# Optimization experiments

Measured on AMD Instinct MI355X. Metric: run time of the kernel, lower is better.

The kernel has to match this reference:

```python
import jax, jax.numpy as jnp
import numpy as np
import jax.lax as lax


def _log_bf_np(z, s2, s0):
    # Bayes factor per feature; s0 is the prior precision tau_0[l,k] (scalar)
    s0_inv = 1.0 / s0
    s2ps0inv = s2 + s0_inv
    return 0.5 * (jnp.log(s2) - jnp.log(s2ps0inv) + z ** 2 * (s0_inv / s2ps0inv))


def setup_inputs() -> dict:
    key = jax.random.key(0)
    ks = jax.random.split(key, 8)
    n, p, z, l = 1000, 50000, 20, 10
    data = jax.random.normal(ks[0], (n, p), jnp.float32)
    mean_z = jax.random.normal(ks[1], (n, z), jnp.float32)
    # factor second moment must be PSD with strictly positive diagonal (E_zzk > 0)
    mean_zz = (mean_z.T @ mean_z) / n + jnp.eye(z, dtype=jnp.float32)
    mean_w = jax.random.normal(ks[2], (l, z, p), jnp.float32) * 0.01
    var_w = jax.random.uniform(ks[3], (l, z), jnp.float32, minval=0.1, maxval=1.0)
    alpha = jax.random.uniform(ks[4], (l, z, p), jnp.float32)
    alpha = alpha / jnp.sum(alpha, axis=-1, keepdims=True)
    tau = jnp.asarray(1.5, jnp.float32)
    tau_0 = jax.random.uniform(ks[5], (l, z), jnp.float32, minval=0.5, maxval=2.0)
    pi = jax.random.uniform(ks[6], (z, p), jnp.float32, minval=0.5, maxval=1.5)
    pi = pi / jnp.sum(pi, axis=-1, keepdims=True)
    return {"data": data, "mean_z": mean_z, "mean_zz": mean_zz, "mean_w": mean_w,
            "var_w": var_w, "alpha": alpha, "tau": tau, "tau_0": tau_0, "pi": pi}


def reference(data, mean_z, mean_zz, mean_w, var_w, alpha, tau, tau_0, pi):
    """LoadingModel.update: sequential CAVI over factors (k) and single effects (l).
    mean_w/alpha: [l, z, p]; var_w/tau_0: [l, z]; pi: [z, p]; data: [n, p]; mean_z: [n, z].
    Returns updated (mean_w, var_w, alpha)."""
    l_dim, z_dim, p_dim = mean_w.shape
    # collapsed loading moments: W[k, :] = sum_l mean_w[l,k,:] * alpha[l,k,:]
    W = jnp.sum(mean_w * alpha, axis=0)            # [z, p]
    ZtX = mean_z.T @ data                           # [z, p] (precompute of mean_z[:,k] @ data)
    log_pi = jnp.log(pi)                            # [z, p]

    def factor_step(carry, kdx):
        W, mean_w, var_w, alpha = carry
        E_zzk = mean_zz[kdx, kdx]
        Wk = W[kdx]                                 # [p]
        # Wnk.T @ E_zpzk over j != k  ==  mean_zz[kdx] @ W - E_zzk * Wk (avoids the gather)
        RtZk = ZtX[kdx] - (mean_zz[kdx] @ W - E_zzk * Wk)   # [p]
        log_pi_k = log_pi[kdx]
        s2_s = 1.0 / (E_zzk * tau)
        zs_scale = jnp.sqrt(E_zzk * tau) / E_zzk

        def effect_step(Wk, xs):
            mw_l, a_l, t0_l = xs                    # [p], [p], scalar
            Wkl = Wk - mw_l * a_l                   # remove effect l from residual fit
            E_RtZk = RtZk - E_zzk * Wkl             # [p]
            var_new = jnp.reciprocal(tau * E_zzk + t0_l)   # scalar
            mean_new = tau * var_new * E_RtZk       # [p]
            Z_s = E_RtZk * zs_scale
            log_bf = _log_bf_np(Z_s, s2_s, t0_l)
            alpha_new = jax.nn.softmax(log_pi_k + log_bf)
            Wk_new = Wkl + mean_new * alpha_new
            return Wk_new, (mean_new, var_new, alpha_new)

        Wk_new, (mw_rows, vw_rows, a_rows) = lax.scan(
            effect_step, Wk, (mean_w[:, kdx, :], alpha[:, kdx, :], tau_0[:, kdx]))
        mean_w = mean_w.at[:, kdx, :].set(mw_rows)
        var_w = var_w.at[:, kdx].set(vw_rows)
        alpha = alpha.at[:, kdx, :].set(a_rows)
        W = W.at[kdx].set(Wk_new)
        return (W, mean_w, var_w, alpha), None

    (W, mean_w, var_w, alpha), _ = lax.scan(
        factor_step, (W, mean_w, var_w, alpha), jnp.arange(z_dim))
    return mean_w, var_w, alpha
```

## Files before the change

kernel.cpp:

```cpp
#include <hip/hip_runtime.h>
#include <stdint.h>


#define NTA 128
#define NBA 398
#define NSZ 4
#define NSW 5
#define PSTRIDE 50944

#define NT_B 1024
#define NWAVE_B 16
#define COLS_B 960
#define NBLK_B 53

constexpr int N_DIM = 1000;
constexpr int P_DIM = 50000;
constexpr int Z_DIM = 20;
constexpr int L_DIM = 10;

static_assert(NTA * NBA == PSTRIDE, "A covers PSTRIDE columns");
static_assert(NBLK_B * COLS_B >= P_DIM, "B covers all real columns");
static_assert(NBLK_B * COLS_B <= PSTRIDE, "B stash reads in bounds");
static_assert(NBLK_B <= 64, "one poll load per lane");

using u64 = unsigned long long;

__device__ __forceinline__ float wred_max(float v) {
#pragma unroll
  for (int m = 32; m; m >>= 1) v = fmaxf(v, __shfl_xor(v, m, 64));
  return v;
}
__device__ __forceinline__ float wred_sum(float v) {
#pragma unroll
  for (int m = 32; m; m >>= 1) v += __shfl_xor(v, m, 64);
  return v;
}

__global__ __launch_bounds__(NTA) void precompute_kernel(
    const float* __restrict__ data,
    const float* __restrict__ mean_z,
    const float* __restrict__ mean_zz,
    const float* __restrict__ mean_w_in,
    const float* __restrict__ alpha_in,
    const float* __restrict__ tau_p,
    const float* __restrict__ tau0,
    float* __restrict__ ztx_stash,
    float* __restrict__ W_stash,
    float* __restrict__ out_vw)
{
  const int bid  = blockIdx.x;
  const int role = bid / NBA;
  const int b2   = bid % NBA;
  const int col  = b2 * NTA + threadIdx.x;
  const bool act = (col < P_DIM);

  if (role == 0 && b2 < 2) {
    int g = b2 * NTA + threadIdx.x;
    if (g < L_DIM * Z_DIM) {
      int k = g % Z_DIM;
      out_vw[g] = 1.0f / (tau_p[0] * mean_zz[k * Z_DIM + k] + tau0[g]);
    }
  }

  if (role < NSZ) {
    const int s  = role;
    const int n0 = s * (N_DIM / NSZ);
    const int n1 = n0 + (N_DIM / NSZ);
    float z[Z_DIM];
#pragma unroll
    for (int k = 0; k < Z_DIM; k++) z[k] = 0.f;
    const float* dcol = data + col;
#pragma unroll 8
    for (int n = n0; n < n1; n++) {
      float d = act ? dcol[(size_t)n * P_DIM] : 0.f;
#pragma unroll
      for (int k = 0; k < Z_DIM; k++) z[k] += mean_z[n * Z_DIM + k] * d;
    }
#pragma unroll
    for (int k = 0; k < Z_DIM; k++)
      ztx_stash[(size_t)(s * Z_DIM + k) * PSTRIDE + col] = z[k];
  } else {
    const int s = role - NSZ;
    float Wp[Z_DIM];
#pragma unroll
    for (int j = 0; j < Z_DIM; j++) Wp[j] = 0.f;
#pragma unroll
    for (int li = 0; li < 2; li++) {
      const int l = 2 * s + li;
#pragma unroll
      for (int j = 0; j < Z_DIM; j++) {
        if (act) {
          size_t idx = ((size_t)(l * Z_DIM + j)) * P_DIM + col;
          Wp[j] += mean_w_in[idx] * alpha_in[idx];
        }
      }
    }
#pragma unroll
    for (int j = 0; j < Z_DIM; j++)
      W_stash[(size_t)(s * Z_DIM + j) * PSTRIDE + col] = Wp[j];
  }
}

__global__ __launch_bounds__(NT_B) void loading_model_seq(
    const float* __restrict__ mean_zz,
    const float* __restrict__ mean_w_in,
    const float* __restrict__ alpha_in,
    const float* __restrict__ tau_p,
    const float* __restrict__ tau0,
    const float* __restrict__ pi,
    const float* __restrict__ ztx_stash,
    const float* __restrict__ W_stash,
    float* __restrict__ out_mw,
    float* __restrict__ out_alpha,
    u64* __restrict__ slots)
{
  const int tid  = threadIdx.x;
  const int blk  = blockIdx.x;
  const int lane = tid & 63;
  const int wid  = tid >> 6;
  const bool work = (wid > 0);
  const int col  = blk * COLS_B + (tid - 64);
  const bool active = work && (col < P_DIM);
  const float tau = tau_p[0];

  __shared__ float lds_wmax[NWAVE_B];
  __shared__ float lds_wsum[NWAVE_B];
  __shared__ float lds_lse;

  float ztx[Z_DIM], W[Z_DIM];
#pragma unroll
  for (int k = 0; k < Z_DIM; k++) ztx[k] = 0.f;
#pragma unroll
  for (int j = 0; j < Z_DIM; j++) W[j] = 0.f;
  if (work) {
#pragma unroll
    for (int s = 0; s < NSZ; s++)
#pragma unroll
      for (int k = 0; k < Z_DIM; k++)
        ztx[k] += ztx_stash[(size_t)(s * Z_DIM + k) * PSTRIDE + col];
#pragma unroll
    for (int s = 0; s < NSW; s++)
#pragma unroll
      for (int j = 0; j < Z_DIM; j++)
        W[j] += W_stash[(size_t)(s * Z_DIM + j) * PSTRIDE + col];
  }

  float pival = active ? pi[col] : 1.0f;
  float mw = 0.f, av = 0.f;
  if (active) { mw = mean_w_in[col]; av = alpha_in[col]; }

  const float E0    = mean_zz[0];
  const float ktau0 = tau * E0;
  float cs2   = 1.0f / ktau0;
  float czsc2 = tau / E0;
  float nc0, nc1, nmnc;
  {
    const float t0    = tau0[0];
    const float s0inv = 1.0f / t0;
    const float s2p   = cs2 + s0inv;
    nc0  = 0.5f * (__logf(cs2) - __logf(s2p));
    nc1  = 0.5f * czsc2 * (s0inv / s2p);
    nmnc = tau / (ktau0 + t0);
  }

#pragma unroll
  for (int k = 0; k < Z_DIM; k++) {
    const float E    = mean_zz[k * Z_DIM + k];
    const float ktau = tau * E;

    float acc = 0.f;
#pragma unroll
    for (int j = 0; j < Z_DIM; j++) acc += mean_zz[k * Z_DIM + j] * W[j];
    const float RtZk = ztx[k] - (acc - E * W[k]);
    const float lpk  = active ? __logf(pival) : -INFINITY;
    if (k + 1 < Z_DIM && active) pival = pi[(size_t)(k + 1) * P_DIM + col];

    float Wk = W[k];
    for (int l = 0; l < L_DIM; l++) {
      const float c0  = nc0;
      const float c1  = nc1;
      const float mnc = nmnc;

      const float Wkl = Wk - mw * av;
      const float E_R = RtZk - E * Wkl;
      const float mean_new = mnc * E_R;
      float logit = lpk + c0 + c1 * E_R * E_R;
      if (!active) logit = -INFINITY;

      const size_t oidx = ((size_t)(l * Z_DIM + k)) * P_DIM + col;
      if (active) out_mw[oidx] = mean_new;

      float wmax = wred_max(logit);
      float ew   = active ? __expf(logit - wmax) : 0.f;
      float wsum = wred_sum(ew);
      if (work && lane == 0) { lds_wmax[wid] = wmax; lds_wsum[wid] = wsum; }
      __syncthreads();

      const int s   = k * L_DIM + l + 1;
      const int buf = s & 1;

      if (wid == 0) {
        const bool val = (lane >= 1 && lane < NWAVE_B);
        float m  = val ? lds_wmax[lane] : -INFINITY;
        float sv = val ? lds_wsum[lane] : 0.f;
        float M  = wred_max(m);
        float S  = wred_sum(val ? __expf(m - M) * sv : 0.f);
        if (lane == 0) {
          float lse_b = M + __logf(S);
          __hip_atomic_store(&slots[buf * NBLK_B + blk],
                             (((u64)(unsigned)s) << 32) | (u64)__float_as_uint(lse_b),
                             __ATOMIC_RELAXED, __HIP_MEMORY_SCOPE_AGENT);
        }
        bool need = (lane < NBLK_B);
        u64 raw = 0;
        while (need) {
          raw = __hip_atomic_load(&slots[buf * NBLK_B + lane],
                                  __ATOMIC_RELAXED, __HIP_MEMORY_SCOPE_AGENT);
          if ((unsigned)(raw >> 32) == (unsigned)s) need = false;
        }
        float bl = (lane < NBLK_B) ? __uint_as_float((unsigned)raw) : -INFINITY;
        float Mg = wred_max(bl);
        float ps = (lane < NBLK_B) ? __expf(bl - Mg) : 0.f;
        float Sg = wred_sum(ps);
        if (lane == 0) lds_lse = Mg + __logf(Sg);
      } else {
        float mw_n = 0.f, av_n = 0.f;
        int ln = l + 1, kn = k;
        if (ln == L_DIM) { ln = 0; kn = k + 1; }
        if (kn < Z_DIM) {
          if (active) {
            size_t idx2 = ((size_t)(ln * Z_DIM + kn)) * P_DIM + col;
            mw_n = mean_w_in[idx2];
            av_n = alpha_in[idx2];
          }
          if (ln == 0) {
            const float En = mean_zz[kn * Z_DIM + kn];
            const float kt = tau * En;
            cs2   = 1.0f / kt;
            czsc2 = tau / En;
          }
          const float t0n   = tau0[ln * Z_DIM + kn];
          const float s0inv = 1.0f / t0n;
          const float s2p   = cs2 + s0inv;
          nc0  = 0.5f * (__logf(cs2) - __logf(s2p));
          nc1  = 0.5f * czsc2 * (s0inv / s2p);
          nmnc = (ln == 0) ? tau / (tau * mean_zz[kn * Z_DIM + kn] + t0n)
                           : tau / (ktau + t0n);
        }
        mw = mw_n;
        av = av_n;
      }
      __syncthreads();

      const float LSEt = lds_lse;
      const float alpha_new = active ? __expf(logit - LSEt) : 0.f;
      Wk = Wkl + mean_new * alpha_new;
      if (active) out_alpha[oidx] = alpha_new;
    }
    W[k] = Wk;
  }
}

extern "C" void kernel_launch(void* const* d_in, const int* in_sizes, int n_in,
                              void* d_out, int out_size, void* d_ws, size_t ws_size,
                              hipStream_t stream) {
  const float* data    = (const float*)d_in[0];
  const float* mean_z  = (const float*)d_in[1];
  const float* mean_zz = (const float*)d_in[2];
  const float* mean_w  = (const float*)d_in[3];
  const float* alpha   = (const float*)d_in[5];
  const float* tau     = (const float*)d_in[6];
  const float* tau0    = (const float*)d_in[7];
  const float* pi      = (const float*)d_in[8];

  float* out_mw    = (float*)d_out;
  float* out_vw    = out_mw + (size_t)L_DIM * Z_DIM * P_DIM;
  float* out_alpha = out_vw + (size_t)L_DIM * Z_DIM;
  u64*   ws        = (u64*)d_ws;

  float* ztx_stash = out_mw;
  float* W_stash   = out_alpha;

  hipMemsetAsync(d_ws, 0, 2 * NBLK_B * sizeof(u64), stream);

  hipLaunchKernelGGL(precompute_kernel, dim3((NSZ + NSW) * NBA), dim3(NTA),
                     0, stream,
                     data, mean_z, mean_zz, mean_w, alpha, tau, tau0,
                     ztx_stash, W_stash, out_vw);

  void* args[] = {(void*)&mean_zz, (void*)&mean_w, (void*)&alpha,
                  (void*)&tau, (void*)&tau0, (void*)&pi,
                  (void*)&ztx_stash, (void*)&W_stash,
                  (void*)&out_mw, (void*)&out_alpha, (void*)&ws};
  hipLaunchCooperativeKernel((void*)loading_model_seq, dim3(NBLK_B),
                             dim3(NT_B), args, 0, stream);
}
```

Measured before the change: 1.161 ms.

## Replace block barriers with tagged LDS flags and a dedicated reducer wave

Wave 0 becomes a persistent reducer. It polls tagged LDS slots holding the per-wave max and sum, combines them, runs the cross-block slot exchange, and publishes the global log-sum-exp through a tagged LDS word. Worker waves no longer call __syncthreads each step; they post their partials, prefetch the next step's inputs and log(pi), then spin on the result word. This removes two block-wide barriers per step from the 200-step sequential chain. In exchange, workers busy-wait on LDS, and correctness depends on relaxed atomics with tags and double buffering staying ordered.

```diff
diff --git a/kernel.cpp b/kernel.cpp
--- a/kernel.cpp
+++ b/kernel.cpp
@@ -17,6 +17,7 @@
 constexpr int P_DIM = 50000;
 constexpr int Z_DIM = 20;
 constexpr int L_DIM = 10;
+constexpr int NSTEP = Z_DIM * L_DIM;
 
 static_assert(NTA * NBA == PSTRIDE, "A covers PSTRIDE columns");
 static_assert(NBLK_B * COLS_B >= P_DIM, "B covers all real columns");
@@ -34,6 +35,9 @@
 #pragma unroll
   for (int m = 32; m; m >>= 1) v += __shfl_xor(v, m, 64);
   return v;
+}
+__device__ __forceinline__ u64 tagpack(int s, float v) {
+  return (((u64)(unsigned)s) << 32) | (u64)__float_as_uint(v);
 }
 
 __global__ __launch_bounds__(NTA) void precompute_kernel(
@@ -118,34 +122,86 @@
   const int blk  = blockIdx.x;
   const int lane = tid & 63;
   const int wid  = tid >> 6;
-  const bool work = (wid > 0);
-  const int col  = blk * COLS_B + (tid - 64);
-  const bool active = work && (col < P_DIM);
   const float tau = tau_p[0];
 
-  __shared__ float lds_wmax[NWAVE_B];
-  __shared__ float lds_wsum[NWAVE_B];
-  __shared__ float lds_lse;
+  __shared__ u64 lds_m[2][NWAVE_B];
+  __shared__ u64 lds_s[2][NWAVE_B];
+  __shared__ u64 lds_res[2];
+
+  if (tid < NWAVE_B) {
+    lds_m[0][tid] = 0; lds_m[1][tid] = 0;
+    lds_s[0][tid] = 0; lds_s[1][tid] = 0;
+  }
+  if (tid == 0) { lds_res[0] = 0; lds_res[1] = 0; }
+  __syncthreads();
+
+  if (wid == 0) {
+    __builtin_amdgcn_s_setprio(1);
+    for (int s = 1; s <= NSTEP; s++) {
+      const int buf = s & 1;
+      const bool val = (lane >= 1 && lane < NWAVE_B);
+      u64 rm = 0, rs = 0;
+      bool nm = val, ns = val;
+      while (nm || ns) {
+        if (nm) {
+          rm = __hip_atomic_load(&lds_m[buf][lane], __ATOMIC_RELAXED,
+                                 __HIP_MEMORY_SCOPE_WORKGROUP);
+          if ((unsigned)(rm >> 32) == (unsigned)s) nm = false;
+        }
+        if (ns) {
+          rs = __hip_atomic_load(&lds_s[buf][lane], __ATOMIC_RELAXED,
+                                 __HIP_MEMORY_SCOPE_WORKGROUP);
+          if ((unsigned)(rs >> 32) == (unsigned)s) ns = false;
+        }
+      }
+      float m  = val ? __uint_as_float((unsigned)rm) : -INFINITY;
+      float sv = val ? __uint_as_float((unsigned)rs) : 0.f;
+      float M  = wred_max(m);
+      float S  = wred_sum(val ? __expf(m - M) * sv : 0.f);
+      if (lane == 0) {
+        float lse_b = M + __logf(S);
+        __hip_atomic_store(&slots[buf * NBLK_B + blk], tagpack(s, lse_b),
+                           __ATOMIC_RELAXED, __HIP_MEMORY_SCOPE_AGENT);
+      }
+      bool need = (lane < NBLK_B);
+      u64 raw = 0;
+      while (need) {
+        raw = __hip_atomic_load(&slots[buf * NBLK_B + lane], __ATOMIC_RELAXED,
+                                __HIP_MEMORY_SCOPE_AGENT);
+        if ((unsigned)(raw >> 32) == (unsigned)s) need = false;
+      }
+      float bl = (lane < NBLK_B) ? __uint_as_float((unsigned)raw) : -INFINITY;
+      float Mg = wred_max(bl);
+      float Sg = wred_sum((lane < NBLK_B) ? __expf(bl - Mg) : 0.f);
+      if (lane == 0)
+        __hip_atomic_store(&lds_res[buf], tagpack(s, Mg + __logf(Sg)),
+                           __ATOMIC_RELAXED, __HIP_MEMORY_SCOPE_WORKGROUP);
+    }
+    return;
+  }
+
+  const int col = blk * COLS_B + (tid - 64);
+  const bool active = (col < P_DIM);
 
   float ztx[Z_DIM], W[Z_DIM];
 #pragma unroll
   for (int k = 0; k < Z_DIM; k++) ztx[k] = 0.f;
 #pragma unroll
   for (int j = 0; j < Z_DIM; j++) W[j] = 0.f;
-  if (work) {
-#pragma unroll
-    for (int s = 0; s < NSZ; s++)
-#pragma unroll
-      for (int k = 0; k < Z_DIM; k++)
-        ztx[k] += ztx_stash[(size_t)(s * Z_DIM + k) * PSTRIDE + col];
-#pragma unroll
-    for (int s = 0; s < NSW; s++)
-#pragma unroll
-      for (int j = 0; j < Z_DIM; j++)
-        W[j] += W_stash[(size_t)(s * Z_DIM + j) * PSTRIDE + col];
-  }
+#pragma unroll
+  for (int s = 0; s < NSZ; s++)
+#pragma unroll
+    for (int k = 0; k < Z_DIM; k++)
+      ztx[k] += ztx_stash[(size_t)(s * Z_DIM + k) * PSTRIDE + col];
+#pragma unroll
+  for (int s = 0; s < NSW; s++)
+#pragma unroll
+    for (int j = 0; j < Z_DIM; j++)
+      W[j] += W_stash[(size_t)(s * Z_DIM + j) * PSTRIDE + col];
 
   float pival = active ? pi[col] : 1.0f;
+  float lpk   = active ? __logf(pival) : -INFINITY;
+  float nlpk  = lpk;
   float mw = 0.f, av = 0.f;
   if (active) { mw = mean_w_in[col]; av = alpha_in[col]; }
 
@@ -172,7 +228,6 @@
 #pragma unroll
     for (int j = 0; j < Z_DIM; j++) acc += mean_zz[k * Z_DIM + j] * W[j];
     const float RtZk = ztx[k] - (acc - E * W[k]);
-    const float lpk  = active ? __logf(pival) : -INFINITY;
     if (k + 1 < Z_DIM && active) pival = pi[(size_t)(k + 1) * P_DIM + col];
 
     float Wk = W[k];
@@ -193,38 +248,17 @@
       float wmax = wred_max(logit);
       float ew   = active ? __expf(logit - wmax) : 0.f;
       float wsum = wred_sum(ew);
-      if (work && lane == 0) { lds_wmax[wid] = wmax; lds_wsum[wid] = wsum; }
-      __syncthreads();
-
       const int s   = k * L_DIM + l + 1;
       const int buf = s & 1;
-
-      if (wid == 0) {
-        const bool val = (lane >= 1 && lane < NWAVE_B);
-        float m  = val ? lds_wmax[lane] : -INFINITY;
-        float sv = val ? lds_wsum[lane] : 0.f;
-        float M  = wred_max(m);
-        float S  = wred_sum(val ? __expf(m - M) * sv : 0.f);
-        if (lane == 0) {
-          float lse_b = M + __logf(S);
-          __hip_atomic_store(&slots[buf * NBLK_B + blk],
-                             (((u64)(unsigned)s) << 32) | (u64)__float_as_uint(lse_b),
-                             __ATOMIC_RELAXED, __HIP_MEMORY_SCOPE_AGENT);
-        }
-        bool need = (lane < NBLK_B);
-        u64 raw = 0;
-        while (need) {
-          raw = __hip_atomic_load(&slots[buf * NBLK_B + lane],
-                                  __ATOMIC_RELAXED, __HIP_MEMORY_SCOPE_AGENT);
-          if ((unsigned)(raw >> 32) == (unsigned)s) need = false;
-        }
-        float bl = (lane < NBLK_B) ? __uint_as_float((unsigned)raw) : -INFINITY;
-        float Mg = wred_max(bl);
-        float ps = (lane < NBLK_B) ? __expf(bl - Mg) : 0.f;
-        float Sg = wred_sum(ps);
-        if (lane == 0) lds_lse = Mg + __logf(Sg);
-      } else {
-        float mw_n = 0.f, av_n = 0.f;
+      if (lane == 0) {
+        __hip_atomic_store(&lds_m[buf][wid], tagpack(s, wmax),
+                           __ATOMIC_RELAXED, __HIP_MEMORY_SCOPE_WORKGROUP);
+        __hip_atomic_store(&lds_s[buf][wid], tagpack(s, wsum),
+                           __ATOMIC_RELAXED, __HIP_MEMORY_SCOPE_WORKGROUP);
+      }
+
+      float mw_n = 0.f, av_n = 0.f;
+      {
         int ln = l + 1, kn = k;
         if (ln == L_DIM) { ln = 0; kn = k + 1; }
         if (kn < Z_DIM) {
@@ -238,6 +272,7 @@
             const float kt = tau * En;
             cs2   = 1.0f / kt;
             czsc2 = tau / En;
+            nlpk  = active ? __logf(pival) : -INFINITY;
           }
           const float t0n   = tau0[ln * Z_DIM + kn];
           const float s0inv = 1.0f / t0n;
@@ -247,17 +282,23 @@
           nmnc = (ln == 0) ? tau / (tau * mean_zz[kn * Z_DIM + kn] + t0n)
                            : tau / (ktau + t0n);
         }
-        mw = mw_n;
-        av = av_n;
-      }
-      __syncthreads();
-
-      const float LSEt = lds_lse;
+      }
+
+      u64 r;
+      do {
+        r = __hip_atomic_load(&lds_res[buf], __ATOMIC_RELAXED,
+                              __HIP_MEMORY_SCOPE_WORKGROUP);
+      } while ((unsigned)(r >> 32) != (unsigned)s);
+      const float LSEt = __uint_as_float((unsigned)r);
+
       const float alpha_new = active ? __expf(logit - LSEt) : 0.f;
       Wk = Wkl + mean_new * alpha_new;
       if (active) out_alpha[oidx] = alpha_new;
+      mw = mw_n;
+      av = av_n;
     }
     W[k] = Wk;
+    lpk  = nlpk;
   }
 }
 
```

Measured after the change: 1.259 ms. +8.5%, slower.

## Cut cooperative grid to 25 blocks with two columns per thread and overlap polling

Applied to the files above, without the earlier changes.

Each thread of the sequential cooperative kernel now handles two columns, and every wave, including wave 0, does column work. This shrinks the grid from 53 to 25 blocks, so each of the 200 grid-wide log-sum-exp exchanges polls fewer slots. The slot publish is moved ahead of the next-step prefetch and the spin-wait after it, so the loads overlap the wait. The ZtX partials are reduced once up front into a scratch zone inside out_mw rather than kept as 20 registers per thread. The cost is more registers per thread, more serial work per block, and a reliance on the out_mw and out_alpha scratch areas not being overwritten too early.

```diff
diff --git a/kernel.cpp b/kernel.cpp
--- a/kernel.cpp
+++ b/kernel.cpp
@@ -10,17 +10,18 @@
 
 #define NT_B 1024
 #define NWAVE_B 16
-#define COLS_B 960
-#define NBLK_B 53
+#define CPT 2
+#define COLS_B (NT_B * CPT)
+#define NBLK_B 25
 
 constexpr int N_DIM = 1000;
 constexpr int P_DIM = 50000;
 constexpr int Z_DIM = 20;
 constexpr int L_DIM = 10;
+constexpr int ZONE_P0 = 160;
 
 static_assert(NTA * NBA == PSTRIDE, "A covers PSTRIDE columns");
 static_assert(NBLK_B * COLS_B >= P_DIM, "B covers all real columns");
-static_assert(NBLK_B * COLS_B <= PSTRIDE, "B stash reads in bounds");
 static_assert(NBLK_B <= 64, "one poll load per lane");
 
 using u64 = unsigned long long;
@@ -34,6 +35,9 @@
 #pragma unroll
   for (int m = 32; m; m >>= 1) v += __shfl_xor(v, m, 64);
   return v;
+}
+__device__ __forceinline__ u64 tagpack(int s, float v) {
+  return (((u64)(unsigned)s) << 32) | (u64)__float_as_uint(v);
 }
 
 __global__ __launch_bounds__(NTA) void precompute_kernel(
@@ -44,7 +48,7 @@
     const float* __restrict__ alpha_in,
     const float* __restrict__ tau_p,
     const float* __restrict__ tau0,
-    float* __restrict__ ztx_stash,
+    float* __restrict__ ztx_part,
     float* __restrict__ W_stash,
     float* __restrict__ out_vw)
 {
@@ -78,7 +82,7 @@
     }
 #pragma unroll
     for (int k = 0; k < Z_DIM; k++)
-      ztx_stash[(size_t)(s * Z_DIM + k) * PSTRIDE + col] = z[k];
+      ztx_part[(size_t)(s * Z_DIM + k) * PSTRIDE + col] = z[k];
   } else {
     const int s = role - NSZ;
     float Wp[Z_DIM];
@@ -108,46 +112,67 @@
     const float* __restrict__ tau_p,
     const float* __restrict__ tau0,
     const float* __restrict__ pi,
-    const float* __restrict__ ztx_stash,
-    const float* __restrict__ W_stash,
-    float* __restrict__ out_mw,
-    float* __restrict__ out_alpha,
+    const float* ztx_part,
+    const float* W_stash,
+    float* zone,
+    float* out_mw,
+    float* out_alpha,
     u64* __restrict__ slots)
 {
   const int tid  = threadIdx.x;
   const int blk  = blockIdx.x;
   const int lane = tid & 63;
   const int wid  = tid >> 6;
-  const bool work = (wid > 0);
-  const int col  = blk * COLS_B + (tid - 64);
-  const bool active = work && (col < P_DIM);
   const float tau = tau_p[0];
+
+  int col[CPT]; bool act[CPT]; int colc[CPT];
+#pragma unroll
+  for (int c = 0; c < CPT; c++) {
+    col[c]  = blk * COLS_B + c * NT_B + tid;
+    act[c]  = (col[c] < P_DIM);
+    colc[c] = act[c] ? col[c] : (P_DIM - 1);
+  }
 
   __shared__ float lds_wmax[NWAVE_B];
   __shared__ float lds_wsum[NWAVE_B];
   __shared__ float lds_lse;
 
-  float ztx[Z_DIM], W[Z_DIM];
-#pragma unroll
-  for (int k = 0; k < Z_DIM; k++) ztx[k] = 0.f;
-#pragma unroll
-  for (int j = 0; j < Z_DIM; j++) W[j] = 0.f;
-  if (work) {
-#pragma unroll
-    for (int s = 0; s < NSZ; s++)
-#pragma unroll
-      for (int k = 0; k < Z_DIM; k++)
-        ztx[k] += ztx_stash[(size_t)(s * Z_DIM + k) * PSTRIDE + col];
-#pragma unroll
-    for (int s = 0; s < NSW; s++)
-#pragma unroll
-      for (int j = 0; j < Z_DIM; j++)
-        W[j] += W_stash[(size_t)(s * Z_DIM + j) * PSTRIDE + col];
-  }
-
-  float pival = active ? pi[col] : 1.0f;
-  float mw = 0.f, av = 0.f;
-  if (active) { mw = mean_w_in[col]; av = alpha_in[col]; }
+  float W[CPT][Z_DIM];
+#pragma unroll
+  for (int c = 0; c < CPT; c++)
+#pragma unroll
+    for (int j = 0; j < Z_DIM; j++) {
+      float w = 0.f;
+#pragma unroll
+      for (int s = 0; s < NSW; s++)
+        w += W_stash[(size_t)(s * Z_DIM + j) * PSTRIDE + colc[c]];
+      W[c][j] = w;
+    }
+
+  float ztxc[CPT];
+#pragma unroll
+  for (int k = 0; k < Z_DIM; k++) {
+#pragma unroll
+    for (int c = 0; c < CPT; c++) {
+      float z = 0.f;
+#pragma unroll
+      for (int s = 0; s < NSZ; s++)
+        z += ztx_part[(size_t)(s * Z_DIM + k) * PSTRIDE + colc[c]];
+      if (k == 0) ztxc[c] = z;
+      else if (act[c]) zone[(size_t)k * P_DIM + col[c]] = z;
+    }
+  }
+
+  float pival[CPT], lpk[CPT], nlpk[CPT];
+  float mw[CPT], av[CPT];
+#pragma unroll
+  for (int c = 0; c < CPT; c++) {
+    pival[c] = pi[colc[c]];
+    lpk[c]   = act[c] ? __logf(pival[c]) : -INFINITY;
+    nlpk[c]  = lpk[c];
+    mw[c] = mean_w_in[colc[c]];
+    av[c] = alpha_in[colc[c]];
+  }
 
   const float E0    = mean_zz[0];
   const float ktau0 = tau * E0;
@@ -163,81 +188,91 @@
     nmnc = tau / (ktau0 + t0);
   }
 
+  float ztxn[CPT] = {0.f, 0.f};
+
 #pragma unroll
   for (int k = 0; k < Z_DIM; k++) {
     const float E    = mean_zz[k * Z_DIM + k];
     const float ktau = tau * E;
 
-    float acc = 0.f;
-#pragma unroll
-    for (int j = 0; j < Z_DIM; j++) acc += mean_zz[k * Z_DIM + j] * W[j];
-    const float RtZk = ztx[k] - (acc - E * W[k]);
-    const float lpk  = active ? __logf(pival) : -INFINITY;
-    if (k + 1 < Z_DIM && active) pival = pi[(size_t)(k + 1) * P_DIM + col];
-
-    float Wk = W[k];
+    float RtZk[CPT];
+#pragma unroll
+    for (int c = 0; c < CPT; c++) {
+      float acc = 0.f;
+#pragma unroll
+      for (int j = 0; j < Z_DIM; j++) acc += mean_zz[k * Z_DIM + j] * W[c][j];
+      RtZk[c] = ztxc[c] - (acc - E * W[c][k]);
+    }
+    if (k + 1 < Z_DIM) {
+#pragma unroll
+      for (int c = 0; c < CPT; c++)
+        pival[c] = pi[(size_t)(k + 1) * P_DIM + colc[c]];
+    }
+
+    float Wk[CPT];
+#pragma unroll
+    for (int c = 0; c < CPT; c++) Wk[c] = W[c][k];
+
     for (int l = 0; l < L_DIM; l++) {
       const float c0  = nc0;
       const float c1  = nc1;
       const float mnc = nmnc;
 
-      const float Wkl = Wk - mw * av;
-      const float E_R = RtZk - E * Wkl;
-      const float mean_new = mnc * E_R;
-      float logit = lpk + c0 + c1 * E_R * E_R;
-      if (!active) logit = -INFINITY;
-
-      const size_t oidx = ((size_t)(l * Z_DIM + k)) * P_DIM + col;
-      if (active) out_mw[oidx] = mean_new;
-
-      float wmax = wred_max(logit);
-      float ew   = active ? __expf(logit - wmax) : 0.f;
+      float Wkl[CPT], mean_new[CPT], logit[CPT];
+#pragma unroll
+      for (int c = 0; c < CPT; c++) {
+        Wkl[c] = Wk[c] - mw[c] * av[c];
+        const float E_R = RtZk[c] - E * Wkl[c];
+        mean_new[c] = mnc * E_R;
+        logit[c] = act[c] ? (lpk[c] + c0 + c1 * E_R * E_R) : -INFINITY;
+        if (act[c])
+          out_mw[((size_t)(l * Z_DIM + k)) * P_DIM + col[c]] = mean_new[c];
+      }
+
+      float lmax = fmaxf(logit[0], logit[1]);
+      float wmax = wred_max(lmax);
+      float ew = 0.f;
+#pragma unroll
+      for (int c = 0; c < CPT; c++)
+        if (act[c]) ew += __expf(logit[c] - wmax);
       float wsum = wred_sum(ew);
-      if (work && lane == 0) { lds_wmax[wid] = wmax; lds_wsum[wid] = wsum; }
+      if (lane == 0) { lds_wmax[wid] = wmax; lds_wsum[wid] = wsum; }
       __syncthreads();
 
       const int s   = k * L_DIM + l + 1;
       const int buf = s & 1;
-
       if (wid == 0) {
-        const bool val = (lane >= 1 && lane < NWAVE_B);
+        const bool val = (lane < NWAVE_B);
         float m  = val ? lds_wmax[lane] : -INFINITY;
         float sv = val ? lds_wsum[lane] : 0.f;
         float M  = wred_max(m);
         float S  = wred_sum(val ? __expf(m - M) * sv : 0.f);
-        if (lane == 0) {
-          float lse_b = M + __logf(S);
+        if (lane == 0)
           __hip_atomic_store(&slots[buf * NBLK_B + blk],
-                             (((u64)(unsigned)s) << 32) | (u64)__float_as_uint(lse_b),
+                             tagpack(s, M + __logf(S)),
                              __ATOMIC_RELAXED, __HIP_MEMORY_SCOPE_AGENT);
-        }
-        bool need = (lane < NBLK_B);
-        u64 raw = 0;
-        while (need) {
-          raw = __hip_atomic_load(&slots[buf * NBLK_B + lane],
-                                  __ATOMIC_RELAXED, __HIP_MEMORY_SCOPE_AGENT);
-          if ((unsigned)(raw >> 32) == (unsigned)s) need = false;
-        }
-        float bl = (lane < NBLK_B) ? __uint_as_float((unsigned)raw) : -INFINITY;
-        float Mg = wred_max(bl);
-        float ps = (lane < NBLK_B) ? __expf(bl - Mg) : 0.f;
-        float Sg = wred_sum(ps);
-        if (lane == 0) lds_lse = Mg + __logf(Sg);
-      } else {
-        float mw_n = 0.f, av_n = 0.f;
+      }
+
+      float mwn[CPT] = {0.f, 0.f}, avn[CPT] = {0.f, 0.f};
+      {
         int ln = l + 1, kn = k;
         if (ln == L_DIM) { ln = 0; kn = k + 1; }
         if (kn < Z_DIM) {
-          if (active) {
-            size_t idx2 = ((size_t)(ln * Z_DIM + kn)) * P_DIM + col;
-            mw_n = mean_w_in[idx2];
-            av_n = alpha_in[idx2];
+#pragma unroll
+          for (int c = 0; c < CPT; c++) {
+            size_t idx2 = ((size_t)(ln * Z_DIM + kn)) * P_DIM + colc[c];
+            mwn[c] = mean_w_in[idx2];
+            avn[c] = alpha_in[idx2];
           }
           if (ln == 0) {
             const float En = mean_zz[kn * Z_DIM + kn];
-            const float kt = tau * En;
-            cs2   = 1.0f / kt;
+            cs2   = 1.0f / (tau * En);
             czsc2 = tau / En;
+#pragma unroll
+            for (int c = 0; c < CPT; c++) {
+              ztxn[c] = zone[(size_t)kn * P_DIM + colc[c]];
+              nlpk[c] = act[c] ? __logf(pival[c]) : -INFINITY;
+            }
           }
           const float t0n   = tau0[ln * Z_DIM + kn];
           const float s0inv = 1.0f / t0n;
@@ -247,17 +282,40 @@
           nmnc = (ln == 0) ? tau / (tau * mean_zz[kn * Z_DIM + kn] + t0n)
                            : tau / (ktau + t0n);
         }
-        mw = mw_n;
-        av = av_n;
+      }
+
+      if (wid == 0) {
+        bool need = (lane < NBLK_B);
+        u64 raw = 0;
+        while (need) {
+          raw = __hip_atomic_load(&slots[buf * NBLK_B + lane], __ATOMIC_RELAXED,
+                                  __HIP_MEMORY_SCOPE_AGENT);
+          if ((unsigned)(raw >> 32) == (unsigned)s) need = false;
+        }
+        float bl = (lane < NBLK_B) ? __uint_as_float((unsigned)raw) : -INFINITY;
+        float Mg = wred_max(bl);
+        float Sg = wred_sum((lane < NBLK_B) ? __expf(bl - Mg) : 0.f);
+        if (lane == 0) lds_lse = Mg + __logf(Sg);
       }
       __syncthreads();
 
       const float LSEt = lds_lse;
-      const float alpha_new = active ? __expf(logit - LSEt) : 0.f;
-      Wk = Wkl + mean_new * alpha_new;
-      if (active) out_alpha[oidx] = alpha_new;
-    }
-    W[k] = Wk;
+#pragma unroll
+      for (int c = 0; c < CPT; c++) {
+        const float alpha_new = act[c] ? __expf(logit[c] - LSEt) : 0.f;
+        Wk[c] = Wkl[c] + mean_new[c] * alpha_new;
+        if (act[c])
+          out_alpha[((size_t)(l * Z_DIM + k)) * P_DIM + col[c]] = alpha_new;
+        mw[c] = mwn[c];
+        av[c] = avn[c];
+      }
+    }
+#pragma unroll
+    for (int c = 0; c < CPT; c++) {
+      W[c][k] = Wk[c];
+      ztxc[c] = ztxn[c];
+      lpk[c]  = nlpk[c];
+    }
   }
 }
 
@@ -278,19 +336,20 @@
   float* out_alpha = out_vw + (size_t)L_DIM * Z_DIM;
   u64*   ws        = (u64*)d_ws;
 
-  float* ztx_stash = out_mw;
   float* W_stash   = out_alpha;
+  float* ztx_part  = out_alpha + (size_t)NSW * Z_DIM * PSTRIDE;
+  float* zone      = out_mw + (size_t)ZONE_P0 * P_DIM;
 
   hipMemsetAsync(d_ws, 0, 2 * NBLK_B * sizeof(u64), stream);
 
   hipLaunchKernelGGL(precompute_kernel, dim3((NSZ + NSW) * NBA), dim3(NTA),
                      0, stream,
                      data, mean_z, mean_zz, mean_w, alpha, tau, tau0,
-                     ztx_stash, W_stash, out_vw);
+                     ztx_part, W_stash, out_vw);
 
   void* args[] = {(void*)&mean_zz, (void*)&mean_w, (void*)&alpha,
                   (void*)&tau, (void*)&tau0, (void*)&pi,
-                  (void*)&ztx_stash, (void*)&W_stash,
+                  (void*)&ztx_part, (void*)&W_stash, (void*)&zone,
                   (void*)&out_mw, (void*)&out_alpha, (void*)&ws};
   hipLaunchCooperativeKernel((void*)loading_model_seq, dim3(NBLK_B),
                              dim3(NT_B), args, 0, stream);
```

Measured after the change: 1.152 ms. No clear change (-0.7%).
